# Performance work log

Measured on AMD Instinct MI355X. Metric: run time of the kernel, lower is better.

Reference implementation:

```python
import jax, jax.numpy as jnp
import numpy as np

B, L, D, H = 2, 2048, 1024, 16
DH = D // H  # 64

def setup_inputs() -> dict:
    key = jax.random.key(0)
    kx, kq, kk, kv, ko = jax.random.split(key, 5)
    s = 1.0 / np.sqrt(D)  # roughly kaiming-uniform scale for Linear weights
    return {
        "x": jax.random.normal(kx, (B, L, D), dtype=jnp.float32),
        "Wq": jax.random.uniform(kq, (D, D), jnp.float32, -s, s),
        "Wk": jax.random.uniform(kk, (D, D), jnp.float32, -s, s),
        "Wv": jax.random.uniform(kv, (D, D), jnp.float32, -s, s),
        "Wo": jax.random.uniform(ko, (D, D), jnp.float32, -s, s),
    }

def reference(x, Wq, Wk, Wv, Wo):
    # torch nn.Linear: y = x @ W.T  (bias disabled, bias_qkv=False)
    def heads(Wt):
        y = jnp.einsum('bld,ed->ble', x, Wt)          # (B, L, D)
        return y.reshape(B, L, H, DH).transpose(0, 2, 1, 3)  # (B, H, L, DH)
    q, k, v = heads(Wq), heads(Wk), heads(Wv)
    scores = jnp.einsum('bhld,bhmd->bhlm', q, k) / jnp.sqrt(jnp.float32(DH))  # (B,H,L,L)
    attn = jax.nn.softmax(scores, axis=-1)            # mask=None path
    out = jnp.einsum('bhlm,bhmd->bhld', attn, v)      # (B, H, L, DH)
    concat = out.transpose(0, 2, 1, 3).reshape(B, L, D)
    output = jnp.einsum('bld,ed->ble', concat, Wo)    # final out-proj, no bias
    return (output, attn)
```

## Files before the change

### kernel.cpp

```cpp
#include <hip/hip_runtime.h>
#include <cstdint>
#include <cstddef>

#define B_ 2
#define L_ 2048
#define D_ 1024
#define H_ 16
#define DH_ 64

typedef unsigned short u16;
typedef __attribute__((ext_vector_type(8))) __bf16 bf16x8;
typedef __attribute__((ext_vector_type(8))) short short8;
typedef __attribute__((ext_vector_type(4))) float floatx4;
typedef __attribute__((ext_vector_type(4))) unsigned short ushort4v;

__device__ __forceinline__ u16 f2bf(float f) {
  union { float f; unsigned u; } v; v.f = f;
  return (u16)((v.u + 0x7FFFu + ((v.u >> 16) & 1u)) >> 16);
}

__device__ __forceinline__ floatx4 mfma16(bf16x8 a, bf16x8 b, floatx4 c) {
  return __builtin_amdgcn_mfma_f32_16x16x32_bf16(a, b, c, 0, 0, 0);
}

__device__ __forceinline__ bf16x8 ldfrag(const u16* p) {
  return *(const bf16x8*)(const void*)p;
}

__device__ __forceinline__ void gload_lds16(const void* g, void* l) {
  __builtin_amdgcn_global_load_lds(
      (__attribute__((address_space(1))) void*)g,
      (__attribute__((address_space(3))) void*)l, 16, 0, 0);
}

__global__ void cvt_bf16_kernel(const float* __restrict__ in, u16* __restrict__ out, int n4) {
  int i = blockIdx.x * 256 + threadIdx.x;
  if (i >= n4) return;
  floatx4 v = ((const floatx4*)in)[i];
  ushort4v o;
#pragma unroll
  for (int j = 0; j < 4; j++) o[j] = f2bf(v[j]);
  ((ushort4v*)out)[i] = o;
}

template <int MODE>
__global__ __launch_bounds__(256) void gemm_bt(const u16* __restrict__ A,
                                               const u16* __restrict__ Bw,
                                               void* __restrict__ outv,
                                               int M, int N, int K) {
  __shared__ __align__(16) u16 As[128 * 32];
  __shared__ __align__(16) u16 Bs[128 * 32];
  const int t = threadIdx.x;
  const int lane = t & 63, w = t >> 6;
  const int wm = w >> 1, wn = w & 1;
  const int q = lane >> 4, c = lane & 15;
  const int nbn = N >> 7;
  const int bm = (int)blockIdx.x / nbn, bn = (int)blockIdx.x % nbn;
  const int m0 = bm << 7, n0 = bn << 7;
  const int rowS = t >> 2;
  const int colB = (t & 3) << 4;

  floatx4 acc[4][4];
#pragma unroll
  for (int i = 0; i < 4; i++)
#pragma unroll
    for (int j = 0; j < 4; j++) acc[i][j] = (floatx4){0.f, 0.f, 0.f, 0.f};

  for (int k0 = 0; k0 < K; k0 += 32) {
    __syncthreads();
#pragma unroll
    for (int ch = 0; ch < 2; ch++) {
      gload_lds16((const char*)(A + (size_t)(m0 + ch * 64 + rowS) * K + k0) + colB,
                  (char*)As + ch * 4096 + t * 16);
      gload_lds16((const char*)(Bw + (size_t)(n0 + ch * 64 + rowS) * K + k0) + colB,
                  (char*)Bs + ch * 4096 + t * 16);
    }
    __syncthreads();
    bf16x8 af[4], bfr[4];
#pragma unroll
    for (int mi = 0; mi < 4; mi++) af[mi] = ldfrag(As + (wm * 64 + mi * 16 + c) * 32 + q * 8);
#pragma unroll
    for (int ni = 0; ni < 4; ni++) bfr[ni] = ldfrag(Bs + (wn * 64 + ni * 16 + c) * 32 + q * 8);
#pragma unroll
    for (int mi = 0; mi < 4; mi++)
#pragma unroll
      for (int ni = 0; ni < 4; ni++)
        acc[mi][ni] = mfma16(af[mi], bfr[ni], acc[mi][ni]);
  }

#pragma unroll
  for (int mi = 0; mi < 4; mi++) {
#pragma unroll
    for (int ni = 0; ni < 4; ni++) {
      const int gnn = n0 + wn * 64 + ni * 16 + c;
#pragma unroll
      for (int r = 0; r < 4; r++) {
        const int gm = m0 + wm * 64 + mi * 16 + q * 4 + r;
        float val = acc[mi][ni][r];
        if (MODE == 2) {
          ((float*)outv)[(size_t)gm * N + gnn] = val;
        } else {
          const int b = gm >> 11, l = gm & 2047;
          const int h = gnn >> 6, dh = gnn & 63;
          if (MODE == 0)
            ((u16*)outv)[(((size_t)(b * H_ + h)) * L_ + l) * DH_ + dh] = f2bf(val);
          else
            ((u16*)outv)[(((size_t)(b * H_ + h)) * DH_ + dh) * L_ + l] = f2bf(val);
        }
      }
    }
  }
}

__global__ __launch_bounds__(256) void attn_softmax(const u16* __restrict__ Qh,
                                                    const u16* __restrict__ Kh,
                                                    float* __restrict__ attn) {
  const int t = threadIdx.x;
  const int lane = t & 63, w = t >> 6;
  const int q = lane >> 4, c = lane & 15;
  const int bh = (int)blockIdx.x >> 7;
  const int mt = (int)blockIdx.x & 127;
  const int row0 = mt << 4;
  const u16* Qp = Qh + (size_t)bh * L_ * DH_;
  const u16* Kp = Kh + (size_t)bh * L_ * DH_;
  float* Ap = attn + (size_t)bh * L_ * L_ + (size_t)row0 * L_;
  const int cbase = w << 9;

  const bf16x8 aq0 = ldfrag(Qp + (row0 + c) * DH_ + q * 8);
  const bf16x8 aq1 = ldfrag(Qp + (row0 + c) * DH_ + 32 + q * 8);

  floatx4 S[32];
#pragma unroll
  for (int ct = 0; ct < 32; ct++) {
    const int n0 = cbase + (ct << 4);
    bf16x8 b0 = ldfrag(Kp + (n0 + c) * DH_ + q * 8);
    bf16x8 b1 = ldfrag(Kp + (n0 + c) * DH_ + 32 + q * 8);
    floatx4 a = (floatx4){0.f, 0.f, 0.f, 0.f};
    a = mfma16(aq0, b0, a);
    a = mfma16(aq1, b1, a);
    S[ct] = a * 0.125f;
  }

  float vmax[4] = {-1e30f, -1e30f, -1e30f, -1e30f};
#pragma unroll
  for (int ct = 0; ct < 32; ct++)
#pragma unroll
    for (int r = 0; r < 4; r++) vmax[r] = fmaxf(vmax[r], S[ct][r]);
#pragma unroll
  for (int m = 1; m < 16; m <<= 1)
#pragma unroll
    for (int r = 0; r < 4; r++) vmax[r] = fmaxf(vmax[r], __shfl_xor(vmax[r], m, 64));

  __shared__ float redm[4][16];
  __shared__ float reds[4][16];
  if (c == 0) {
#pragma unroll
    for (int r = 0; r < 4; r++) redm[w][q * 4 + r] = vmax[r];
  }
  __syncthreads();
  float rmax[4];
#pragma unroll
  for (int r = 0; r < 4; r++)
    rmax[r] = fmaxf(fmaxf(redm[0][q * 4 + r], redm[1][q * 4 + r]),
                    fmaxf(redm[2][q * 4 + r], redm[3][q * 4 + r]));

  float vsum[4] = {0.f, 0.f, 0.f, 0.f};
#pragma unroll
  for (int ct = 0; ct < 32; ct++)
#pragma unroll
    for (int r = 0; r < 4; r++) {
      float e = __expf(S[ct][r] - rmax[r]);
      S[ct][r] = e;
      vsum[r] += e;
    }
#pragma unroll
  for (int m = 1; m < 16; m <<= 1)
#pragma unroll
    for (int r = 0; r < 4; r++) vsum[r] += __shfl_xor(vsum[r], m, 64);
  if (c == 0) {
#pragma unroll
    for (int r = 0; r < 4; r++) reds[w][q * 4 + r] = vsum[r];
  }
  __syncthreads();
  float inv[4];
#pragma unroll
  for (int r = 0; r < 4; r++)
    inv[r] = 1.0f / (reds[0][q * 4 + r] + reds[1][q * 4 + r] +
                     reds[2][q * 4 + r] + reds[3][q * 4 + r]);

#pragma unroll
  for (int ct = 0; ct < 32; ct++) {
    const int n0 = cbase + (ct << 4);
#pragma unroll
    for (int r = 0; r < 4; r++)
      Ap[(size_t)(q * 4 + r) * L_ + n0 + c] = S[ct][r] * inv[r];
  }
}

__global__ __launch_bounds__(256) void pv_gemm(const float* __restrict__ P,
                                               const u16* __restrict__ Vt,
                                               u16* __restrict__ concat) {
  const int t = threadIdx.x;
  const int lane = t & 63, w = t >> 6;
  const int q = lane >> 4, c = lane & 15;
  const int bh = (int)blockIdx.x >> 5;
  const int rt = (int)blockIdx.x & 31;
  const int m0 = (rt << 6) + (w << 4);
  const float* Pp = P + (size_t)bh * L_ * L_;
  const u16* Vp = Vt + (size_t)bh * DH_ * L_;
  const int b = bh >> 4, h = bh & 15;

  floatx4 acc[4];
#pragma unroll
  for (int nt = 0; nt < 4; nt++) acc[nt] = (floatx4){0.f, 0.f, 0.f, 0.f};

  for (int k0 = 0; k0 < L_; k0 += 32) {
    const float* pr = Pp + (size_t)(m0 + c) * L_ + k0 + q * 8;
    floatx4 p0 = *(const floatx4*)pr;
    floatx4 p1 = *(const floatx4*)(pr + 4);
    short8 sa;
#pragma unroll
    for (int j = 0; j < 4; j++) sa[j] = (short)f2bf(p0[j]);
#pragma unroll
    for (int j = 0; j < 4; j++) sa[4 + j] = (short)f2bf(p1[j]);
    bf16x8 a = __builtin_bit_cast(bf16x8, sa);
#pragma unroll
    for (int nt = 0; nt < 4; nt++) {
      bf16x8 bfr = ldfrag(Vp + (size_t)(nt * 16 + c) * L_ + k0 + q * 8);
      acc[nt] = mfma16(a, bfr, acc[nt]);
    }
  }

#pragma unroll
  for (int nt = 0; nt < 4; nt++) {
    const int dh = nt * 16 + c;
#pragma unroll
    for (int r = 0; r < 4; r++) {
      const int l = m0 + q * 4 + r;
      concat[((size_t)(b * L_ + l)) * D_ + h * DH_ + dh] = f2bf(acc[nt][r]);
    }
  }
}

extern "C" void kernel_launch(void* const* d_in, const int* in_sizes, int n_in,
                              void* d_out, int out_size, void* d_ws, size_t ws_size,
                              hipStream_t stream) {
  const float* x = (const float*)d_in[0];
  const float* Wq = (const float*)d_in[1];
  const float* Wk = (const float*)d_in[2];
  const float* Wv = (const float*)d_in[3];
  const float* Wo = (const float*)d_in[4];
  float* out = (float*)d_out;

  char* ws = (char*)d_ws;
  u16* xb = (u16*)(ws + 0);
  u16* wqb = (u16*)(ws + 8388608);
  u16* wkb = (u16*)(ws + 10485760);
  u16* wvb = (u16*)(ws + 12582912);
  u16* wob = (u16*)(ws + 14680064);
  u16* Qh = (u16*)(ws + 16777216);
  u16* Kh = (u16*)(ws + 25165824);
  u16* Vt = (u16*)(ws + 33554432);
  u16* concat = (u16*)(ws + 41943040);

  const int MK = B_ * L_ * D_;
  const int WK = D_ * D_;
  cvt_bf16_kernel<<<MK / 4 / 256, 256, 0, stream>>>(x, xb, MK / 4);
  cvt_bf16_kernel<<<WK / 4 / 256, 256, 0, stream>>>(Wq, wqb, WK / 4);
  cvt_bf16_kernel<<<WK / 4 / 256, 256, 0, stream>>>(Wk, wkb, WK / 4);
  cvt_bf16_kernel<<<WK / 4 / 256, 256, 0, stream>>>(Wv, wvb, WK / 4);
  cvt_bf16_kernel<<<WK / 4 / 256, 256, 0, stream>>>(Wo, wob, WK / 4);

  const int M = B_ * L_, N = D_, K = D_;
  const int gblk = (M / 128) * (N / 128);
  gemm_bt<0><<<gblk, 256, 0, stream>>>(xb, wqb, (void*)Qh, M, N, K);
  gemm_bt<0><<<gblk, 256, 0, stream>>>(xb, wkb, (void*)Kh, M, N, K);
  gemm_bt<1><<<gblk, 256, 0, stream>>>(xb, wvb, (void*)Vt, M, N, K);

  float* attn = out + (size_t)B_ * L_ * D_;
  attn_softmax<<<B_ * H_ * (L_ / 16), 256, 0, stream>>>(Qh, Kh, attn);
  pv_gemm<<<B_ * H_ * (L_ / 64), 256, 0, stream>>>(attn, Vt, concat);
  gemm_bt<2><<<gblk, 256, 0, stream>>>(concat, wob, (void*)out, M, N, K);
}
```

Baseline: 997.6 us.

## Fuse PV product into softmax kernel and batch QKV projections into one launch

The PV matmul now runs inside the softmax kernel using the normalized probabilities still held in registers. They are staged as bf16 through per-wave shared memory, and partial outputs from the four waves are summed in shared memory. This removes the re-read of the full fp32 attention matrix (B*H*L*L floats) by a separate pv_gemm kernel. Separately, the Q, K and V projections are merged into a single launch with a 3x larger grid. The fused kernel uses more shared memory and registers, which may lower occupancy.

After: 947.0 us. -5.1%, faster.

```diff
diff --git a/kernel.cpp b/kernel.cpp
--- a/kernel.cpp
+++ b/kernel.cpp
@@ -112,19 +112,99 @@
   }
 }
 
-__global__ __launch_bounds__(256) void attn_softmax(const u16* __restrict__ Qh,
-                                                    const u16* __restrict__ Kh,
-                                                    float* __restrict__ attn) {
+__global__ __launch_bounds__(256) void gemm_qkv(const u16* __restrict__ A,
+                                                const u16* __restrict__ Wq,
+                                                const u16* __restrict__ Wk,
+                                                const u16* __restrict__ Wv,
+                                                u16* __restrict__ Qh,
+                                                u16* __restrict__ Kh,
+                                                u16* __restrict__ Vt) {
+  const int K = D_, N = D_;
+  __shared__ __align__(16) u16 As[128 * 32];
+  __shared__ __align__(16) u16 Bs[128 * 32];
+  const int t = threadIdx.x;
+  const int lane = t & 63, w = t >> 6;
+  const int wm = w >> 1, wn = w & 1;
+  const int q = lane >> 4, c = lane & 15;
+  const int bid = (int)blockIdx.x;
+  const int bm = bid / 24, bnall = bid % 24;
+  const int which = bnall >> 3, bn = bnall & 7;
+  const u16* Bw = (which == 0) ? Wq : ((which == 1) ? Wk : Wv);
+  u16* outp = (which == 0) ? Qh : ((which == 1) ? Kh : Vt);
+  const int m0 = bm << 7, n0 = bn << 7;
+  const int rowS = t >> 2;
+  const int colB = (t & 3) << 4;
+
+  floatx4 acc[4][4];
+#pragma unroll
+  for (int i = 0; i < 4; i++)
+#pragma unroll
+    for (int j = 0; j < 4; j++) acc[i][j] = (floatx4){0.f, 0.f, 0.f, 0.f};
+
+  for (int k0 = 0; k0 < K; k0 += 32) {
+    __syncthreads();
+#pragma unroll
+    for (int ch = 0; ch < 2; ch++) {
+      gload_lds16((const char*)(A + (size_t)(m0 + ch * 64 + rowS) * K + k0) + colB,
+                  (char*)As + ch * 4096 + t * 16);
+      gload_lds16((const char*)(Bw + (size_t)(n0 + ch * 64 + rowS) * K + k0) + colB,
+                  (char*)Bs + ch * 4096 + t * 16);
+    }
+    __syncthreads();
+    bf16x8 af[4], bfr[4];
+#pragma unroll
+    for (int mi = 0; mi < 4; mi++) af[mi] = ldfrag(As + (wm * 64 + mi * 16 + c) * 32 + q * 8);
+#pragma unroll
+    for (int ni = 0; ni < 4; ni++) bfr[ni] = ldfrag(Bs + (wn * 64 + ni * 16 + c) * 32 + q * 8);
+#pragma unroll
+    for (int mi = 0; mi < 4; mi++)
+#pragma unroll
+      for (int ni = 0; ni < 4; ni++)
+        acc[mi][ni] = mfma16(af[mi], bfr[ni], acc[mi][ni]);
+  }
+
+#pragma unroll
+  for (int mi = 0; mi < 4; mi++) {
+#pragma unroll
+    for (int ni = 0; ni < 4; ni++) {
+      const int gnn = n0 + wn * 64 + ni * 16 + c;
+#pragma unroll
+      for (int r = 0; r < 4; r++) {
+        const int gm = m0 + wm * 64 + mi * 16 + q * 4 + r;
+        float val = acc[mi][ni][r];
+        const int b = gm >> 11, l = gm & 2047;
+        const int h = gnn >> 6, dh = gnn & 63;
+        if (which < 2)
+          outp[(((size_t)(b * H_ + h)) * L_ + l) * DH_ + dh] = f2bf(val);
+        else
+          outp[(((size_t)(b * H_ + h)) * DH_ + dh) * L_ + l] = f2bf(val);
+      }
+    }
+  }
+}
+
+__global__ __launch_bounds__(256, 2) void attn_fused(const u16* __restrict__ Qh,
+                                                     const u16* __restrict__ Kh,
+                                                     const u16* __restrict__ Vt,
+                                                     float* __restrict__ attn,
+                                                     u16* __restrict__ concat) {
   const int t = threadIdx.x;
   const int lane = t & 63, w = t >> 6;
   const int q = lane >> 4, c = lane & 15;
   const int bh = (int)blockIdx.x >> 7;
   const int mt = (int)blockIdx.x & 127;
   const int row0 = mt << 4;
+  const int b = bh >> 4, h = bh & 15;
   const u16* Qp = Qh + (size_t)bh * L_ * DH_;
   const u16* Kp = Kh + (size_t)bh * L_ * DH_;
+  const u16* Vp = Vt + (size_t)bh * DH_ * L_;
   float* Ap = attn + (size_t)bh * L_ * L_ + (size_t)row0 * L_;
   const int cbase = w << 9;
+
+  __shared__ float redm[4][16];
+  __shared__ float reds[4][16];
+  __shared__ __align__(16) u16 Ps[4][2][16 * 40];
+  __shared__ float Ored[4][16][66];
 
   const bf16x8 aq0 = ldfrag(Qp + (row0 + c) * DH_ + q * 8);
   const bf16x8 aq1 = ldfrag(Qp + (row0 + c) * DH_ + 32 + q * 8);
@@ -151,8 +231,6 @@
 #pragma unroll
     for (int r = 0; r < 4; r++) vmax[r] = fmaxf(vmax[r], __shfl_xor(vmax[r], m, 64));
 
-  __shared__ float redm[4][16];
-  __shared__ float reds[4][16];
   if (c == 0) {
 #pragma unroll
     for (int r = 0; r < 4; r++) redm[w][q * 4 + r] = vmax[r];
@@ -189,57 +267,59 @@
                      reds[2][q * 4 + r] + reds[3][q * 4 + r]);
 
 #pragma unroll
+  for (int ct = 0; ct < 32; ct++)
+#pragma unroll
+    for (int r = 0; r < 4; r++) S[ct][r] *= inv[r];
+
+#pragma unroll
   for (int ct = 0; ct < 32; ct++) {
     const int n0 = cbase + (ct << 4);
 #pragma unroll
     for (int r = 0; r < 4; r++)
-      Ap[(size_t)(q * 4 + r) * L_ + n0 + c] = S[ct][r] * inv[r];
-  }
-}
-
-__global__ __launch_bounds__(256) void pv_gemm(const float* __restrict__ P,
-                                               const u16* __restrict__ Vt,
-                                               u16* __restrict__ concat) {
-  const int t = threadIdx.x;
-  const int lane = t & 63, w = t >> 6;
-  const int q = lane >> 4, c = lane & 15;
-  const int bh = (int)blockIdx.x >> 5;
-  const int rt = (int)blockIdx.x & 31;
-  const int m0 = (rt << 6) + (w << 4);
-  const float* Pp = P + (size_t)bh * L_ * L_;
-  const u16* Vp = Vt + (size_t)bh * DH_ * L_;
-  const int b = bh >> 4, h = bh & 15;
-
-  floatx4 acc[4];
-#pragma unroll
-  for (int nt = 0; nt < 4; nt++) acc[nt] = (floatx4){0.f, 0.f, 0.f, 0.f};
-
-  for (int k0 = 0; k0 < L_; k0 += 32) {
-    const float* pr = Pp + (size_t)(m0 + c) * L_ + k0 + q * 8;
-    floatx4 p0 = *(const floatx4*)pr;
-    floatx4 p1 = *(const floatx4*)(pr + 4);
-    short8 sa;
-#pragma unroll
-    for (int j = 0; j < 4; j++) sa[j] = (short)f2bf(p0[j]);
-#pragma unroll
-    for (int j = 0; j < 4; j++) sa[4 + j] = (short)f2bf(p1[j]);
-    bf16x8 a = __builtin_bit_cast(bf16x8, sa);
+      Ap[(size_t)(q * 4 + r) * L_ + n0 + c] = S[ct][r];
+  }
+
+  floatx4 oacc[4];
+#pragma unroll
+  for (int nt = 0; nt < 4; nt++) oacc[nt] = (floatx4){0.f, 0.f, 0.f, 0.f};
+
+#pragma unroll
+  for (int cp = 0; cp < 16; cp++) {
+    u16* Pb = Ps[w][cp & 1];
+#pragma unroll
+    for (int dd = 0; dd < 2; dd++)
+#pragma unroll
+      for (int r = 0; r < 4; r++)
+        Pb[(q * 4 + r) * 40 + dd * 16 + c] = f2bf(S[2 * cp + dd][r]);
+    bf16x8 a = ldfrag(Pb + c * 40 + q * 8);
+    const int key0 = cbase + cp * 32;
 #pragma unroll
     for (int nt = 0; nt < 4; nt++) {
-      bf16x8 bfr = ldfrag(Vp + (size_t)(nt * 16 + c) * L_ + k0 + q * 8);
-      acc[nt] = mfma16(a, bfr, acc[nt]);
-    }
-  }
-
-#pragma unroll
-  for (int nt = 0; nt < 4; nt++) {
-    const int dh = nt * 16 + c;
-#pragma unroll
-    for (int r = 0; r < 4; r++) {
-      const int l = m0 + q * 4 + r;
-      concat[((size_t)(b * L_ + l)) * D_ + h * DH_ + dh] = f2bf(acc[nt][r]);
-    }
-  }
+      bf16x8 bfr = ldfrag(Vp + (size_t)(nt * 16 + c) * L_ + key0 + q * 8);
+      oacc[nt] = mfma16(a, bfr, oacc[nt]);
+    }
+  }
+
+#pragma unroll
+  for (int nt = 0; nt < 4; nt++)
+#pragma unroll
+    for (int r = 0; r < 4; r++)
+      Ored[w][q * 4 + r][nt * 16 + c] = oacc[nt][r];
+  __syncthreads();
+
+  const int row = t >> 4;
+  const int dh0 = (t & 15) << 2;
+  float s0 = 0.f, s1 = 0.f, s2 = 0.f, s3 = 0.f;
+#pragma unroll
+  for (int ww = 0; ww < 4; ww++) {
+    s0 += Ored[ww][row][dh0 + 0];
+    s1 += Ored[ww][row][dh0 + 1];
+    s2 += Ored[ww][row][dh0 + 2];
+    s3 += Ored[ww][row][dh0 + 3];
+  }
+  ushort4v o;
+  o[0] = f2bf(s0); o[1] = f2bf(s1); o[2] = f2bf(s2); o[3] = f2bf(s3);
+  *(ushort4v*)&concat[((size_t)(b * L_ + row0 + row)) * D_ + h * DH_ + dh0] = o;
 }
 
 extern "C" void kernel_launch(void* const* d_in, const int* in_sizes, int n_in,
@@ -272,13 +352,11 @@
   cvt_bf16_kernel<<<WK / 4 / 256, 256, 0, stream>>>(Wo, wob, WK / 4);
 
   const int M = B_ * L_, N = D_, K = D_;
-  const int gblk = (M / 128) * (N / 128);
-  gemm_bt<0><<<gblk, 256, 0, stream>>>(xb, wqb, (void*)Qh, M, N, K);
-  gemm_bt<0><<<gblk, 256, 0, stream>>>(xb, wkb, (void*)Kh, M, N, K);
-  gemm_bt<1><<<gblk, 256, 0, stream>>>(xb, wvb, (void*)Vt, M, N, K);
+
+  gemm_qkv<<<(M / 128) * 24, 256, 0, stream>>>(xb, wqb, wkb, wvb, Qh, Kh, Vt);
 
   float* attn = out + (size_t)B_ * L_ * D_;
-  attn_softmax<<<B_ * H_ * (L_ / 16), 256, 0, stream>>>(Qh, Kh, attn);
-  pv_gemm<<<B_ * H_ * (L_ / 64), 256, 0, stream>>>(attn, Vt, concat);
-  gemm_bt<2><<<gblk, 256, 0, stream>>>(concat, wob, (void*)out, M, N, K);
-}
+  attn_fused<<<B_ * H_ * (L_ / 16), 256, 0, stream>>>(Qh, Kh, Vt, attn, concat);
+
+  gemm_bt<2><<<(M / 128) * (N / 128), 256, 0, stream>>>(concat, wob, (void*)out, M, N, K);
+}
```
